# Kernel optimization log

Hardware: AMD Instinct MI355X
Metric: run time of the kernel (lower is better)

Reference implementation:

```python
import jax, jax.numpy as jnp
import numpy as np

B, S, E, G, O, TOPK = 4, 2048, 1024, 8, 4096, 2


def setup_inputs() -> dict:
    key = jax.random.key(0)
    k1, k2, k3, k4 = jax.random.split(key, 4)
    return {
        "hidden_states": jax.random.normal(k1, (B, S, E), dtype=jnp.float32),
        "WG": jax.random.normal(k2, (E, G), dtype=jnp.float32) * (1.0 / np.sqrt(E)),
        "Wi": jax.random.normal(k3, (G, E, O), dtype=jnp.float32) * (1.0 / np.sqrt(E)),
        "down": jax.random.normal(k4, (O, E), dtype=jnp.float32) * (1.0 / np.sqrt(O)),
        "topk": TOPK,
    }


def reference(hidden_states, WG, Wi, down, topk):
    # gate logits: [b, s, g]
    gate = jnp.matmul(hidden_states, WG)
    # sparse path (smoe_fwd): topk mask zeroes non-selected gate LOGITS,
    # so non-selected experts get sigmoid(0) = 0.5 (faithful to source).
    _, idx = jax.lax.top_k(gate, topk)              # [b, s, topk]
    mask = jnp.max(jax.nn.one_hot(idx, gate.shape[-1], dtype=gate.dtype), axis=-2)  # [b, s, g]
    w = jax.nn.sigmoid(gate * mask)                  # [b, s, g]
    # weighted combination over all expert matrices: [b, s, o]
    y = jnp.einsum('bse,bsg,geo->bso', hidden_states, w, Wi)
    # squared ReLU
    h = jnp.square(jax.nn.relu(y))
    return jnp.matmul(h, down)                       # [b, s, e]
```

## Files before the change

kernel.cpp:

```cpp
#include <hip/hip_runtime.h>
#include <hip/hip_bf16.h>
#include <math.h>

typedef __bf16 bf16;
typedef __bf16 bf16x4 __attribute__((ext_vector_type(4)));
typedef __bf16 bf16x8 __attribute__((ext_vector_type(8)));
typedef float  floatx4 __attribute__((ext_vector_type(4)));

#define N_TOK 8192
#define E_DIM 1024
#define G_DIM 8
#define O_DIM 4096
#define EPI_LD 132

__device__ __forceinline__ void gload_lds16(const void* g, void* l) {
    __builtin_amdgcn_global_load_lds(
        (__attribute__((address_space(1))) void*)(g),
        (__attribute__((address_space(3))) void*)(l),
        16, 0, 0);
}

__global__ __launch_bounds__(256) void gate_compute(
    const float* __restrict__ X,
    const float* __restrict__ WG,
    int* __restrict__ sel,
    float* __restrict__ sval)
{
    __shared__ float lwgT[G_DIM * E_DIM];
    const int tid  = threadIdx.x;
    const int wave = tid >> 6;
    const int lane = tid & 63;

#pragma unroll
    for (int k = 0; k < 8; ++k) {
        const int i = k * 256 + tid;
        const float4 v = *(const float4*)(WG + i * 4);
        const int e  = i >> 1;
        const int g0 = (i & 1) * 4;
        lwgT[(g0 + 0) * E_DIM + e] = v.x;
        lwgT[(g0 + 1) * E_DIM + e] = v.y;
        lwgT[(g0 + 2) * E_DIM + e] = v.z;
        lwgT[(g0 + 3) * E_DIM + e] = v.w;
    }
    __syncthreads();

    const int t = blockIdx.x * 4 + wave;
    float acc[G_DIM];
#pragma unroll
    for (int g = 0; g < G_DIM; ++g) acc[g] = 0.f;

#pragma unroll
    for (int it = 0; it < 4; ++it) {
        const int e0 = it * 256 + lane * 4;
        const float4 xv = *(const float4*)(X + (long)t * E_DIM + e0);
#pragma unroll
        for (int g = 0; g < G_DIM; ++g) {
            const float4 wv = *(const float4*)(lwgT + g * E_DIM + e0);
            acc[g] += xv.x * wv.x + xv.y * wv.y + xv.z * wv.z + xv.w * wv.w;
        }
    }
#pragma unroll
    for (int g = 0; g < G_DIM; ++g) {
        float v = acc[g];
#pragma unroll
        for (int off = 32; off > 0; off >>= 1) v += __shfl_down(v, off, 64);
        acc[g] = v;
    }
    if (lane == 0) {
        int i1 = 0;
#pragma unroll
        for (int g = 1; g < G_DIM; ++g) if (acc[g] > acc[i1]) i1 = g;
        int i2 = (i1 == 0) ? 1 : 0;
#pragma unroll
        for (int g = 0; g < G_DIM; ++g)
            if (g != i1 && g != i2 && acc[g] > acc[i2]) i2 = g;
#pragma unroll
        for (int s = 0; s < 2; ++s) {
            const int g = s ? i2 : i1;
            sel[t * 2 + s]  = g;
            sval[t * 2 + s] = 1.f / (1.f + expf(-acc[g])) - 0.5f;
        }
    }
}

__global__ __launch_bounds__(1024) void route_kernel(
    const int* __restrict__ sel, const float* __restrict__ sval,
    int* __restrict__ cnt, int* __restrict__ off, int* __restrict__ offp,
    int* __restrict__ tok, float* __restrict__ scl, int* __restrict__ pos)
{
    __shared__ int hcnt[16][G_DIM];
    __shared__ int wbase[16][G_DIM];
    const int tid  = threadIdx.x;
    const int w    = tid >> 6;
    const int lane = tid & 63;
    const unsigned long long below = ((unsigned long long)1 << lane) - 1;

    int c0[G_DIM];
#pragma unroll
    for (int g = 0; g < G_DIM; ++g) c0[g] = 0;
    for (int c = 0; c < 16; ++c) {
        const int g = sel[w * 1024 + c * 64 + lane];
#pragma unroll
        for (int gg = 0; gg < G_DIM; ++gg)
            c0[gg] += __popcll(__ballot(g == gg));
    }
    if (lane == 0)
#pragma unroll
        for (int g = 0; g < G_DIM; ++g) hcnt[w][g] = c0[g];
    __syncthreads();

    if (tid == 0) {
        int tot[G_DIM];
#pragma unroll
        for (int g = 0; g < G_DIM; ++g) {
            int a = 0;
            for (int ww = 0; ww < 16; ++ww) { wbase[ww][g] = a; a += hcnt[ww][g]; }
            tot[g] = a; cnt[g] = a;
        }
        int a = 0, b = 0;
#pragma unroll
        for (int g = 0; g < G_DIM; ++g) {
            off[g]  = a; a += tot[g];
            offp[g] = b; b += (tot[g] + 127) & ~127;
        }
        offp[G_DIM] = b;
    }
    __syncthreads();

    int run[G_DIM];
#pragma unroll
    for (int g = 0; g < G_DIM; ++g) run[g] = 0;
    for (int c = 0; c < 16; ++c) {
        const int idx = w * 1024 + c * 64 + lane;
        const int g   = sel[idx];
        const float sv = sval[idx];
        int myrank = 0;
#pragma unroll
        for (int gg = 0; gg < G_DIM; ++gg) {
            const unsigned long long m = __ballot(g == gg);
            const int r = run[gg] + __popcll(m & below);
            if (g == gg) myrank = r;
            run[gg] += __popcll(m);
        }
        const int p = wbase[w][g] + myrank;
        tok[g * N_TOK + p] = idx >> 1;
        scl[g * N_TOK + p] = sv;
        pos[idx] = (g << 16) | p;
    }
}

__global__ __launch_bounds__(256) void convert_x(
    const float* __restrict__ X, bf16* __restrict__ Xb)
{
    const long i = ((long)blockIdx.x * 256 + threadIdx.x) * 4;
    const float4 v = *(const float4*)(X + i);
    bf16x4 o;
    o[0] = (bf16)v.x; o[1] = (bf16)v.y; o[2] = (bf16)v.z; o[3] = (bf16)v.w;
    *(bf16x4*)(Xb + i) = o;
}

__global__ __launch_bounds__(256) void transpose_conv(
    const float* __restrict__ S, bf16* __restrict__ D, int R, int C)
{
    __shared__ float tile[64][65];
    const int r0  = blockIdx.x * 64;
    const int c0  = blockIdx.y * 64;
    const int tid = threadIdx.x;
    const int tr  = tid >> 4;
    const int tc4 = (tid & 15) * 4;

#pragma unroll
    for (int p = 0; p < 4; ++p) {
        const int r = p * 16 + tr;
        const float4 v = *(const float4*)(S + (long)(r0 + r) * C + c0 + tc4);
        tile[r][tc4 + 0] = v.x;
        tile[r][tc4 + 1] = v.y;
        tile[r][tc4 + 2] = v.z;
        tile[r][tc4 + 3] = v.w;
    }
    __syncthreads();
#pragma unroll
    for (int p = 0; p < 4; ++p) {
        const int c = p * 16 + tr;
        bf16x4 o;
        o[0] = (bf16)tile[tc4 + 0][c];
        o[1] = (bf16)tile[tc4 + 1][c];
        o[2] = (bf16)tile[tc4 + 2][c];
        o[3] = (bf16)tile[tc4 + 3][c];
        *(bf16x4*)(D + (long)(c0 + c) * R + r0 + tc4) = o;
    }
}

__global__ __launch_bounds__(256) void wsum_kernel(
    const bf16* __restrict__ WiT, bf16* __restrict__ WsumT)
{
    const int o  = blockIdx.x;
    const int e4 = threadIdx.x * 4;
    float a0 = 0.f, a1 = 0.f, a2 = 0.f, a3 = 0.f;
#pragma unroll
    for (int g = 0; g < G_DIM; ++g) {
        const bf16x4 v = *(const bf16x4*)(WiT + (long)o * 8192 + g * E_DIM + e4);
        a0 += (float)v[0]; a1 += (float)v[1]; a2 += (float)v[2]; a3 += (float)v[3];
    }
    bf16x4 w;
    w[0] = (bf16)(0.5f * a0); w[1] = (bf16)(0.5f * a1);
    w[2] = (bf16)(0.5f * a2); w[3] = (bf16)(0.5f * a3);
    *(bf16x4*)(WsumT + (long)o * E_DIM + e4) = w;
}

__global__ __launch_bounds__(128) void gather_rows(
    const bf16* __restrict__ Xb, const int* __restrict__ cnt,
    const int* __restrict__ offp, const int* __restrict__ tok,
    bf16* __restrict__ Xs)
{
    const int slot = blockIdx.x;
    if (slot >= offp[G_DIM]) return;
    int g = 0;
    while (slot >= offp[g + 1]) ++g;
    const int p = slot - offp[g];
    bf16* dst = Xs + (long)slot * E_DIM + threadIdx.x * 8;
    if (p < cnt[g]) {
        const bf16* src = Xb + (long)tok[g * N_TOK + p] * E_DIM + threadIdx.x * 8;
        *(bf16x8*)dst = *(const bf16x8*)src;
    } else {
        bf16x8 z = {};
        *(bf16x8*)dst = z;
    }
}

template <typename OUT, bool VEC>
__global__ __launch_bounds__(256, 4) void gemm_mt(
    const bf16* __restrict__ A, int lda,
    const bf16* __restrict__ BT, int ldb,
    OUT* __restrict__ C, int ldc, int K)
{
    __shared__ char smem[VEC ? (128 * EPI_LD * 2) : 16384];
    bf16* As = (bf16*)smem;
    bf16* Bs = (bf16*)(smem + 8192);

    const int u   = blockIdx.x;
    const int xcd = u & 7;
    const int s   = u >> 3;
    const int mt  = s & 63;
    const int col = xcd + 8 * (s >> 6);

    const int tid  = threadIdx.x;
    const int wave = tid >> 6;
    const int lane = tid & 63;
    const int row0 = mt * 128;
    const int col0 = col * 128;

    const int sr = lane >> 2;
    const int sc = (lane & 3) * 8;
    const bf16* agp0 = A  + (long)(row0 + 16 * wave       + sr) * lda + sc;
    const bf16* agp1 = A  + (long)(row0 + 16 * (wave + 4) + sr) * lda + sc;
    const bf16* bgp0 = BT + (long)(col0 + 16 * wave       + sr) * ldb + sc;
    const bf16* bgp1 = BT + (long)(col0 + 16 * (wave + 4) + sr) * ldb + sc;
    bf16* asl0 = As + (long)wave * 512;
    bf16* asl1 = As + (long)(wave + 4) * 512;
    bf16* bsl0 = Bs + (long)wave * 512;
    bf16* bsl1 = Bs + (long)(wave + 4) * 512;

    const int mi_base = (wave >> 1) * 64;
    const int ni_base = (wave & 1) * 64;
    const int fr = lane & 15;
    const int fq = lane >> 4;

    floatx4 acc[4][4] = {};

    for (int k0 = 0; k0 < K; k0 += 32) {
        __syncthreads();
        gload_lds16(agp0 + k0, (void*)asl0);
        gload_lds16(agp1 + k0, (void*)asl1);
        gload_lds16(bgp0 + k0, (void*)bsl0);
        gload_lds16(bgp1 + k0, (void*)bsl1);
        __syncthreads();

        bf16x8 af[4], bfr[4];
#pragma unroll
        for (int i = 0; i < 4; ++i) {
            af[i]  = *(const bf16x8*)(As + (mi_base + i * 16 + fr) * 32 + fq * 8);
            bfr[i] = *(const bf16x8*)(Bs + (ni_base + i * 16 + fr) * 32 + fq * 8);
        }
#pragma unroll
        for (int i = 0; i < 4; ++i)
#pragma unroll
            for (int j = 0; j < 4; ++j)
                acc[i][j] = __builtin_amdgcn_mfma_f32_16x16x32_bf16(
                    af[i], bfr[j], acc[i][j], 0, 0, 0);
    }

    if (VEC) {
        __syncthreads();
        bf16* tile = (bf16*)smem;
#pragma unroll
        for (int i = 0; i < 4; ++i)
#pragma unroll
            for (int j = 0; j < 4; ++j)
#pragma unroll
                for (int r = 0; r < 4; ++r) {
                    const int rl = mi_base + i * 16 + fq * 4 + r;
                    const int cl = ni_base + j * 16 + fr;
                    tile[rl * EPI_LD + cl] = (bf16)acc[i][j][r];
                }
        __syncthreads();
#pragma unroll
        for (int k = 0; k < 8; ++k) {
            const int rl = (tid >> 3) + 32 * (k >> 1);
            const int cl = (tid & 7) * 8 + 64 * (k & 1);
            const bf16x8 v = *(const bf16x8*)(tile + rl * EPI_LD + cl);
            *(bf16x8*)((bf16*)C + (long)(row0 + rl) * ldc + col0 + cl) = v;
        }
    } else {
#pragma unroll
        for (int i = 0; i < 4; ++i)
#pragma unroll
            for (int j = 0; j < 4; ++j)
#pragma unroll
                for (int r = 0; r < 4; ++r) {
                    const long row = row0 + mi_base + i * 16 + fq * 4 + r;
                    const long cg  = col0 + ni_base + j * 16 + fr;
                    C[row * ldc + cg] = (OUT)acc[i][j][r];
                }
    }
}

__global__ __launch_bounds__(256, 4) void gemm_sparse(
    const bf16* __restrict__ Xs,
    const bf16* __restrict__ WiT,
    const int* __restrict__ cnt,
    const int* __restrict__ off,
    const int* __restrict__ offp,
    const float* __restrict__ scl,
    bf16* __restrict__ ysp)
{
    const int u    = blockIdx.x;
    const int xcd  = u & 7;
    const int s    = u >> 3;
    const int mt   = s & 63;
    const int pair = xcd + 8 * (s >> 6);
    const int g    = pair & 7;
    const int col  = pair >> 3;

    const int cg   = cnt[g];
    const int cgp  = offp[g + 1] - offp[g];
    const int m0   = mt * 128;
    if (m0 >= cgp) return;

    __shared__ char smem[128 * EPI_LD * 2];
    bf16* As = (bf16*)smem;
    bf16* Bs = (bf16*)(smem + 8192);

    const int tid  = threadIdx.x;
    const int wave = tid >> 6;
    const int lane = tid & 63;
    const int col0 = col * 128;

    const int sr = lane >> 2;
    const int sc = (lane & 3) * 8;
    const bf16* A = Xs + (long)(offp[g] + m0) * E_DIM;
    const bf16* agp0 = A + (long)(16 * wave       + sr) * E_DIM + sc;
    const bf16* agp1 = A + (long)(16 * (wave + 4) + sr) * E_DIM + sc;
    const bf16* bgp0 = WiT + (long)(col0 + 16 * wave       + sr) * 8192 + g * E_DIM + sc;
    const bf16* bgp1 = WiT + (long)(col0 + 16 * (wave + 4) + sr) * 8192 + g * E_DIM + sc;
    bf16* asl0 = As + (long)wave * 512;
    bf16* asl1 = As + (long)(wave + 4) * 512;
    bf16* bsl0 = Bs + (long)wave * 512;
    bf16* bsl1 = Bs + (long)(wave + 4) * 512;

    const int mi_base = (wave >> 1) * 64;
    const int ni_base = (wave & 1) * 64;
    const int fr = lane & 15;
    const int fq = lane >> 4;

    floatx4 acc[4][4] = {};

    for (int k0 = 0; k0 < E_DIM; k0 += 32) {
        __syncthreads();
        gload_lds16(agp0 + k0, (void*)asl0);
        gload_lds16(agp1 + k0, (void*)asl1);
        gload_lds16(bgp0 + k0, (void*)bsl0);
        gload_lds16(bgp1 + k0, (void*)bsl1);
        __syncthreads();

        bf16x8 af[4], bfr[4];
#pragma unroll
        for (int i = 0; i < 4; ++i) {
            af[i]  = *(const bf16x8*)(As + (mi_base + i * 16 + fr) * 32 + fq * 8);
            bfr[i] = *(const bf16x8*)(Bs + (ni_base + i * 16 + fr) * 32 + fq * 8);
        }
#pragma unroll
        for (int i = 0; i < 4; ++i)
#pragma unroll
            for (int j = 0; j < 4; ++j)
                acc[i][j] = __builtin_amdgcn_mfma_f32_16x16x32_bf16(
                    af[i], bfr[j], acc[i][j], 0, 0, 0);
    }

    const float* sclg = scl + g * N_TOK;
    const int cl = cg - 1;
    __syncthreads();
    bf16* tile = (bf16*)smem;
#pragma unroll
    for (int i = 0; i < 4; ++i) {
#pragma unroll
        for (int r = 0; r < 4; ++r) {
            const int rl = mi_base + i * 16 + fq * 4 + r;
            const int gm = m0 + rl;
            const float sv = sclg[gm > cl ? cl : gm];
#pragma unroll
            for (int j = 0; j < 4; ++j) {
                const int clc = ni_base + j * 16 + fr;
                tile[rl * EPI_LD + clc] = (bf16)(sv * acc[i][j][r]);
            }
        }
    }
    __syncthreads();
    const long obase = off[g] + m0;
#pragma unroll
    for (int k = 0; k < 8; ++k) {
        const int rl = (tid >> 3) + 32 * (k >> 1);
        const int cc = (tid & 7) * 8 + 64 * (k & 1);
        if (m0 + rl < cg) {
            const bf16x8 v = *(const bf16x8*)(tile + rl * EPI_LD + cc);
            *(bf16x8*)(ysp + (obase + rl) * O_DIM + col0 + cc) = v;
        }
    }
}

__global__ __launch_bounds__(256) void relu2_gather(
    const bf16* __restrict__ Yb,
    const bf16* __restrict__ ysp,
    const int* __restrict__ pos,
    const int* __restrict__ off,
    bf16* __restrict__ H)
{
    const int t  = blockIdx.x;
    const int p0 = pos[t * 2];
    const int p1 = pos[t * 2 + 1];
    const long r0 = off[p0 >> 16] + (p0 & 0xffff);
    const long r1 = off[p1 >> 16] + (p1 & 0xffff);
    const int c = threadIdx.x * 16;

    const bf16* yb = Yb + (long)t * O_DIM + c;
    const bf16* s0 = ysp + r0 * O_DIM + c;
    const bf16* s1 = ysp + r1 * O_DIM + c;
    bf16* hp = H + (long)t * O_DIM + c;

#pragma unroll
    for (int h = 0; h < 2; ++h) {
        const bf16x8 a = *(const bf16x8*)(yb + h * 8);
        const bf16x8 b = *(const bf16x8*)(s0 + h * 8);
        const bf16x8 d = *(const bf16x8*)(s1 + h * 8);
        bf16x8 o;
#pragma unroll
        for (int k = 0; k < 8; ++k) {
            float v = (float)a[k] + (float)b[k] + (float)d[k];
            v = fmaxf(v, 0.f);
            o[k] = (bf16)(v * v);
        }
        *(bf16x8*)(hp + h * 8) = o;
    }
}

extern "C" void kernel_launch(void* const* d_in, const int* in_sizes, int n_in,
                              void* d_out, int out_size, void* d_ws, size_t ws_size,
                              hipStream_t stream)
{
    const float* X  = (const float*)d_in[0];
    const float* WG = (const float*)d_in[1];
    const float* Wi = (const float*)d_in[2];
    const float* dn = (const float*)d_in[3];
    float* out = (float*)d_out;

    char* ws = (char*)d_ws;
    const long MB = 1l << 20;
    int*   cnt   = (int*)ws;
    int*   off   = (int*)(ws + 1024);
    int*   offp  = (int*)(ws + 2048);
    int*   pos   = (int*)(ws + 4096);
    int*   tok   = (int*)(ws + 128 * 1024);
    float* scl   = (float*)(ws + 448 * 1024);
    int*   sel   = (int*)(ws + 704 * 1024);
    float* sval  = (float*)(ws + 768 * 1024);
    bf16*  dnT   = (bf16*)(ws + 1 * MB);
    bf16*  WiT   = (bf16*)(ws + 9 * MB);
    bf16*  Hh    = (bf16*)(ws + 9 * MB);
    bf16*  Xs    = (bf16*)(ws + 73 * MB);
    bf16*  Yb    = (bf16*)(ws + 107 * MB);
    bf16*  ysp   = (bf16*)(ws + 171 * MB);
    bf16*  Xb    = (bf16*)(ws + 171 * MB);
    bf16*  WsumT = (bf16*)(ws + 187 * MB);

    gate_compute<<<dim3(N_TOK / 4), dim3(256), 0, stream>>>(X, WG, sel, sval);
    route_kernel<<<dim3(1), dim3(1024), 0, stream>>>(sel, sval, cnt, off, offp,
                                                     tok, scl, pos);
    convert_x<<<dim3(N_TOK * E_DIM / 1024), dim3(256), 0, stream>>>(X, Xb);
    transpose_conv<<<dim3(8192 / 64, O_DIM / 64), dim3(256), 0, stream>>>(Wi, WiT, 8192, O_DIM);
    transpose_conv<<<dim3(O_DIM / 64, E_DIM / 64), dim3(256), 0, stream>>>(dn, dnT, O_DIM, E_DIM);
    wsum_kernel<<<dim3(O_DIM), dim3(256), 0, stream>>>(WiT, WsumT);
    gemm_mt<bf16, true><<<dim3(64 * 32), dim3(256), 0, stream>>>(
        Xb, E_DIM, WsumT, E_DIM, Yb, O_DIM, E_DIM);
    gather_rows<<<dim3(17408), dim3(128), 0, stream>>>(Xb, cnt, offp, tok, Xs);
    gemm_sparse<<<dim3(G_DIM * 64 * 32), dim3(256), 0, stream>>>(
        Xs, WiT, cnt, off, offp, scl, ysp);
    relu2_gather<<<dim3(N_TOK), dim3(256), 0, stream>>>(Yb, ysp, pos, off, Hh);
    gemm_mt<float, false><<<dim3(64 * 8), dim3(256), 0, stream>>>(
        Hh, O_DIM, dnT, O_DIM, out, E_DIM, O_DIM);
}
```

Measured before the change: 733.7 us.

## Use 256x256 double-buffered swizzled GEMM core for dense and sparse expert matmuls

Replaces the 128x128 single-buffered GEMM tiles for the dense weighted-sum matmul and the per-expert sparse matmul with a shared 256x256 tile core. The core uses 512 threads, 64-wide K steps, XOR-swizzled LDS, and double-buffered global-to-LDS loads issued two tiles ahead. It also raises MFMA issue priority. This targets the low data reuse and the per-step barrier stalls of the old kernels. The cost is 128KB of LDS per block and fewer resident blocks, and sparse groups now pad to 256-row tiles, which wastes more work on partial tiles.

```diff
diff --git a/kernel.cpp b/kernel.cpp
--- a/kernel.cpp
+++ b/kernel.cpp
@@ -228,6 +228,238 @@
     }
 }
 
+__device__ __forceinline__ void gemm_core256(
+    const bf16* __restrict__ Ap, long lda,
+    const bf16* __restrict__ Bp, long ldb,
+    int K, char* smem, floatx4 (&acc)[8][4])
+{
+    const int tid  = threadIdx.x;
+    const int wave = tid >> 6;
+    const int lane = tid & 63;
+    const int wm   = wave >> 2;
+    const int wn   = wave & 3;
+    const int fr   = lane & 15;
+    const int fq   = lane >> 4;
+
+#pragma unroll
+    for (int i = 0; i < 8; ++i)
+#pragma unroll
+        for (int j = 0; j < 4; ++j)
+            acc[i][j] = (floatx4){0.f, 0.f, 0.f, 0.f};
+
+    const int  srow = tid >> 3;
+    const int  ssw  = ((tid & 7) * 16) ^ ((srow & 7) << 4);
+    const char* sa  = (const char*)Ap + (long)srow * (lda * 2) + ssw;
+    const char* sb  = (const char*)Bp + (long)srow * (ldb * 2) + ssw;
+    const long a64  = lda * 128;
+    const long b64  = ldb * 128;
+    char* const lw  = smem + wave * 1024;
+
+#define STAGE256(buf, kt) do {                                              \
+        const long _ko = (long)(kt) * 128;                                  \
+        char* _lb = lw + (buf) * 65536;                                     \
+        _Pragma("unroll")                                                   \
+        for (int _c = 0; _c < 4; ++_c) {                                    \
+            gload_lds16(sa + _ko + _c * a64, _lb + _c * 8192);              \
+            gload_lds16(sb + _ko + _c * b64, _lb + 32768 + _c * 8192);      \
+        }                                                                   \
+    } while (0)
+
+    const int xsw  = (fr & 7) << 4;
+    const int ko0  = (fq * 16) ^ xsw;
+    const int ko1  = (fq * 16 + 64) ^ xsw;
+    const int aoff = (wm * 128 + fr) * 128;
+    const int boff = 32768 + (wn * 64 + fr) * 128;
+
+    const int nt = K >> 6;
+    STAGE256(0, 0);
+    STAGE256(1, 1);
+    asm volatile("s_waitcnt vmcnt(8)" ::: "memory");
+    __builtin_amdgcn_s_barrier();
+    __builtin_amdgcn_sched_barrier(0);
+
+    bf16x8 af[4][2], bv[2][2];
+
+    for (int t = 0; t < nt; ++t) {
+        const char* base = smem + ((t & 1) << 16);
+
+#pragma unroll
+        for (int i = 0; i < 4; ++i) {
+            af[i][0] = *(const bf16x8*)(base + aoff + i * 2048 + ko0);
+            af[i][1] = *(const bf16x8*)(base + aoff + i * 2048 + ko1);
+        }
+#pragma unroll
+        for (int j = 0; j < 2; ++j) {
+            bv[j][0] = *(const bf16x8*)(base + boff + j * 2048 + ko0);
+            bv[j][1] = *(const bf16x8*)(base + boff + j * 2048 + ko1);
+        }
+        __builtin_amdgcn_s_setprio(1);
+#pragma unroll
+        for (int i = 0; i < 4; ++i)
+#pragma unroll
+            for (int j = 0; j < 2; ++j) {
+                acc[i][j] = __builtin_amdgcn_mfma_f32_16x16x32_bf16(af[i][0], bv[j][0], acc[i][j], 0, 0, 0);
+                acc[i][j] = __builtin_amdgcn_mfma_f32_16x16x32_bf16(af[i][1], bv[j][1], acc[i][j], 0, 0, 0);
+            }
+        __builtin_amdgcn_s_setprio(0);
+
+#pragma unroll
+        for (int j = 0; j < 2; ++j) {
+            bv[j][0] = *(const bf16x8*)(base + boff + 4096 + j * 2048 + ko0);
+            bv[j][1] = *(const bf16x8*)(base + boff + 4096 + j * 2048 + ko1);
+        }
+        __builtin_amdgcn_s_setprio(1);
+#pragma unroll
+        for (int i = 0; i < 4; ++i)
+#pragma unroll
+            for (int j = 0; j < 2; ++j) {
+                acc[i][2 + j] = __builtin_amdgcn_mfma_f32_16x16x32_bf16(af[i][0], bv[j][0], acc[i][2 + j], 0, 0, 0);
+                acc[i][2 + j] = __builtin_amdgcn_mfma_f32_16x16x32_bf16(af[i][1], bv[j][1], acc[i][2 + j], 0, 0, 0);
+            }
+        __builtin_amdgcn_s_setprio(0);
+
+#pragma unroll
+        for (int i = 0; i < 4; ++i) {
+            af[i][0] = *(const bf16x8*)(base + aoff + 8192 + i * 2048 + ko0);
+            af[i][1] = *(const bf16x8*)(base + aoff + 8192 + i * 2048 + ko1);
+        }
+        __builtin_amdgcn_s_setprio(1);
+#pragma unroll
+        for (int i = 0; i < 4; ++i)
+#pragma unroll
+            for (int j = 0; j < 2; ++j) {
+                acc[4 + i][2 + j] = __builtin_amdgcn_mfma_f32_16x16x32_bf16(af[i][0], bv[j][0], acc[4 + i][2 + j], 0, 0, 0);
+                acc[4 + i][2 + j] = __builtin_amdgcn_mfma_f32_16x16x32_bf16(af[i][1], bv[j][1], acc[4 + i][2 + j], 0, 0, 0);
+            }
+        __builtin_amdgcn_s_setprio(0);
+
+#pragma unroll
+        for (int j = 0; j < 2; ++j) {
+            bv[j][0] = *(const bf16x8*)(base + boff + j * 2048 + ko0);
+            bv[j][1] = *(const bf16x8*)(base + boff + j * 2048 + ko1);
+        }
+        __builtin_amdgcn_s_setprio(1);
+#pragma unroll
+        for (int i = 0; i < 4; ++i)
+#pragma unroll
+            for (int j = 0; j < 2; ++j) {
+                acc[4 + i][j] = __builtin_amdgcn_mfma_f32_16x16x32_bf16(af[i][0], bv[j][0], acc[4 + i][j], 0, 0, 0);
+                acc[4 + i][j] = __builtin_amdgcn_mfma_f32_16x16x32_bf16(af[i][1], bv[j][1], acc[4 + i][j], 0, 0, 0);
+            }
+        __builtin_amdgcn_s_setprio(0);
+
+        __builtin_amdgcn_sched_barrier(0);
+        __builtin_amdgcn_s_barrier();
+        if (t + 2 < nt) {
+            STAGE256(t & 1, t + 2);
+            asm volatile("s_waitcnt vmcnt(8)" ::: "memory");
+        } else {
+            asm volatile("s_waitcnt vmcnt(0)" ::: "memory");
+        }
+        __builtin_amdgcn_s_barrier();
+        __builtin_amdgcn_sched_barrier(0);
+    }
+#undef STAGE256
+}
+
+__global__ __launch_bounds__(512, 2) void gemm256_base(
+    const bf16* __restrict__ A, const bf16* __restrict__ BT,
+    bf16* __restrict__ C)
+{
+    __shared__ __align__(16) char smem[131072];
+    const int u   = blockIdx.x;
+    const int xcd = u & 7;
+    const int s   = u >> 3;
+    const int mt  = s & 31;
+    const int ct  = xcd + 8 * (s >> 5);
+    const int row0 = mt * 256, col0 = ct * 256;
+
+    floatx4 acc[8][4];
+    gemm_core256(A + (long)row0 * E_DIM, E_DIM,
+                 BT + (long)col0 * E_DIM, E_DIM,
+                 E_DIM, smem, acc);
+
+    const int tid = threadIdx.x, wave = tid >> 6, lane = tid & 63;
+    const int wm = wave >> 2, wn = wave & 3, fr = lane & 15, fq = lane >> 4;
+    bf16* tile = (bf16*)smem;
+#pragma unroll
+    for (int i = 0; i < 8; ++i)
+#pragma unroll
+        for (int j = 0; j < 4; ++j)
+#pragma unroll
+            for (int r = 0; r < 4; ++r)
+                tile[(wm * 128 + i * 16 + fq * 4 + r) * 256 + wn * 64 + j * 16 + fr] =
+                    (bf16)(acc[i][j][r]);
+    __syncthreads();
+#pragma unroll
+    for (int k = 0; k < 16; ++k) {
+        const int rl = (tid >> 5) + k * 16;
+        const int cc = (tid & 31) * 8;
+        *(bf16x8*)(C + (long)(row0 + rl) * O_DIM + col0 + cc) =
+            *(const bf16x8*)(tile + rl * 256 + cc);
+    }
+}
+
+__global__ __launch_bounds__(512, 2) void gemm256_sparse(
+    const bf16* __restrict__ Xs,
+    const bf16* __restrict__ WiT,
+    const int* __restrict__ cnt,
+    const int* __restrict__ off,
+    const int* __restrict__ offp,
+    const float* __restrict__ scl,
+    bf16* __restrict__ ysp)
+{
+    const int u   = blockIdx.x;
+    const int xcd = u & 7;
+    const int s   = u >> 3;
+    const int mt  = s & 63;
+    const int pc  = xcd + 8 * (s >> 6);
+    const int g   = pc & 7;
+    const int ct  = pc >> 3;
+
+    const int cg     = cnt[g];
+    const int base_p = offp[g];
+    const int cgp    = offp[g + 1] - base_p;
+    const int m0     = mt * 256;
+    if (m0 >= cgp) return;
+
+    __shared__ __align__(16) char smem[131072];
+    const int col0 = ct * 256;
+
+    floatx4 acc[8][4];
+    gemm_core256(Xs + (long)(base_p + m0) * E_DIM, E_DIM,
+                 WiT + (long)col0 * 8192 + g * E_DIM, 8192,
+                 E_DIM, smem, acc);
+
+    const int tid = threadIdx.x, wave = tid >> 6, lane = tid & 63;
+    const int wm = wave >> 2, wn = wave & 3, fr = lane & 15, fq = lane >> 4;
+    const float* sclg = scl + g * N_TOK;
+    const int clmax = cg - 1;
+    bf16* tile = (bf16*)smem;
+#pragma unroll
+    for (int i = 0; i < 8; ++i)
+#pragma unroll
+        for (int r = 0; r < 4; ++r) {
+            const int rl = wm * 128 + i * 16 + fq * 4 + r;
+            const int gm = m0 + rl;
+            const float sv = sclg[gm > clmax ? clmax : gm];
+#pragma unroll
+            for (int j = 0; j < 4; ++j)
+                tile[rl * 256 + wn * 64 + j * 16 + fr] = (bf16)(sv * acc[i][j][r]);
+        }
+    __syncthreads();
+    const long ob = off[g] + m0;
+#pragma unroll
+    for (int k = 0; k < 16; ++k) {
+        const int rl = (tid >> 5) + k * 16;
+        if (m0 + rl < cg) {
+            const int cc = (tid & 31) * 8;
+            *(bf16x8*)(ysp + (ob + rl) * O_DIM + col0 + cc) =
+                *(const bf16x8*)(tile + rl * 256 + cc);
+        }
+    }
+}
+
 template <typename OUT, bool VEC>
 __global__ __launch_bounds__(256, 4) void gemm_mt(
     const bf16* __restrict__ A, int lda,
@@ -322,109 +554,6 @@
                     const long cg  = col0 + ni_base + j * 16 + fr;
                     C[row * ldc + cg] = (OUT)acc[i][j][r];
                 }
-    }
-}
-
-__global__ __launch_bounds__(256, 4) void gemm_sparse(
-    const bf16* __restrict__ Xs,
-    const bf16* __restrict__ WiT,
-    const int* __restrict__ cnt,
-    const int* __restrict__ off,
-    const int* __restrict__ offp,
-    const float* __restrict__ scl,
-    bf16* __restrict__ ysp)
-{
-    const int u    = blockIdx.x;
-    const int xcd  = u & 7;
-    const int s    = u >> 3;
-    const int mt   = s & 63;
-    const int pair = xcd + 8 * (s >> 6);
-    const int g    = pair & 7;
-    const int col  = pair >> 3;
-
-    const int cg   = cnt[g];
-    const int cgp  = offp[g + 1] - offp[g];
-    const int m0   = mt * 128;
-    if (m0 >= cgp) return;
-
-    __shared__ char smem[128 * EPI_LD * 2];
-    bf16* As = (bf16*)smem;
-    bf16* Bs = (bf16*)(smem + 8192);
-
-    const int tid  = threadIdx.x;
-    const int wave = tid >> 6;
-    const int lane = tid & 63;
-    const int col0 = col * 128;
-
-    const int sr = lane >> 2;
-    const int sc = (lane & 3) * 8;
-    const bf16* A = Xs + (long)(offp[g] + m0) * E_DIM;
-    const bf16* agp0 = A + (long)(16 * wave       + sr) * E_DIM + sc;
-    const bf16* agp1 = A + (long)(16 * (wave + 4) + sr) * E_DIM + sc;
-    const bf16* bgp0 = WiT + (long)(col0 + 16 * wave       + sr) * 8192 + g * E_DIM + sc;
-    const bf16* bgp1 = WiT + (long)(col0 + 16 * (wave + 4) + sr) * 8192 + g * E_DIM + sc;
-    bf16* asl0 = As + (long)wave * 512;
-    bf16* asl1 = As + (long)(wave + 4) * 512;
-    bf16* bsl0 = Bs + (long)wave * 512;
-    bf16* bsl1 = Bs + (long)(wave + 4) * 512;
-
-    const int mi_base = (wave >> 1) * 64;
-    const int ni_base = (wave & 1) * 64;
-    const int fr = lane & 15;
-    const int fq = lane >> 4;
-
-    floatx4 acc[4][4] = {};
-
-    for (int k0 = 0; k0 < E_DIM; k0 += 32) {
-        __syncthreads();
-        gload_lds16(agp0 + k0, (void*)asl0);
-        gload_lds16(agp1 + k0, (void*)asl1);
-        gload_lds16(bgp0 + k0, (void*)bsl0);
-        gload_lds16(bgp1 + k0, (void*)bsl1);
-        __syncthreads();
-
-        bf16x8 af[4], bfr[4];
-#pragma unroll
-        for (int i = 0; i < 4; ++i) {
-            af[i]  = *(const bf16x8*)(As + (mi_base + i * 16 + fr) * 32 + fq * 8);
-            bfr[i] = *(const bf16x8*)(Bs + (ni_base + i * 16 + fr) * 32 + fq * 8);
-        }
-#pragma unroll
-        for (int i = 0; i < 4; ++i)
-#pragma unroll
-            for (int j = 0; j < 4; ++j)
-                acc[i][j] = __builtin_amdgcn_mfma_f32_16x16x32_bf16(
-                    af[i], bfr[j], acc[i][j], 0, 0, 0);
-    }
-
-    const float* sclg = scl + g * N_TOK;
-    const int cl = cg - 1;
-    __syncthreads();
-    bf16* tile = (bf16*)smem;
-#pragma unroll
-    for (int i = 0; i < 4; ++i) {
-#pragma unroll
-        for (int r = 0; r < 4; ++r) {
-            const int rl = mi_base + i * 16 + fq * 4 + r;
-            const int gm = m0 + rl;
-            const float sv = sclg[gm > cl ? cl : gm];
-#pragma unroll
-            for (int j = 0; j < 4; ++j) {
-                const int clc = ni_base + j * 16 + fr;
-                tile[rl * EPI_LD + clc] = (bf16)(sv * acc[i][j][r]);
-            }
-        }
-    }
-    __syncthreads();
-    const long obase = off[g] + m0;
-#pragma unroll
-    for (int k = 0; k < 8; ++k) {
-        const int rl = (tid >> 3) + 32 * (k >> 1);
-        const int cc = (tid & 7) * 8 + 64 * (k & 1);
-        if (m0 + rl < cg) {
-            const bf16x8 v = *(const bf16x8*)(tile + rl * EPI_LD + cc);
-            *(bf16x8*)(ysp + (obase + rl) * O_DIM + col0 + cc) = v;
-        }
     }
 }
 
@@ -499,10 +628,9 @@
     transpose_conv<<<dim3(8192 / 64, O_DIM / 64), dim3(256), 0, stream>>>(Wi, WiT, 8192, O_DIM);
     transpose_conv<<<dim3(O_DIM / 64, E_DIM / 64), dim3(256), 0, stream>>>(dn, dnT, O_DIM, E_DIM);
     wsum_kernel<<<dim3(O_DIM), dim3(256), 0, stream>>>(WiT, WsumT);
-    gemm_mt<bf16, true><<<dim3(64 * 32), dim3(256), 0, stream>>>(
-        Xb, E_DIM, WsumT, E_DIM, Yb, O_DIM, E_DIM);
+    gemm256_base<<<dim3(512), dim3(512), 0, stream>>>(Xb, WsumT, Yb);
     gather_rows<<<dim3(17408), dim3(128), 0, stream>>>(Xb, cnt, offp, tok, Xs);
-    gemm_sparse<<<dim3(G_DIM * 64 * 32), dim3(256), 0, stream>>>(
+    gemm256_sparse<<<dim3(8192), dim3(512), 0, stream>>>(
         Xs, WiT, cnt, off, offp, scl, ysp);
     relu2_gather<<<dim3(N_TOK), dim3(256), 0, stream>>>(Yb, ysp, pos, off, Hh);
     gemm_mt<float, false><<<dim3(64 * 8), dim3(256), 0, stream>>>(
```

Measured after the change: 742.4 us. Within noise of the previous version (+1.2%).
